# Kernel optimization log

Measured on AMD Instinct MI355X. Metric: run time of the kernel, lower is better.

## Reference

```python
import jax, jax.numpy as jnp
import numpy as np


def setup_inputs() -> dict:
    key = jax.random.key(0)
    k1, k2, k3 = jax.random.split(key, 3)
    C, H, W = 64, 512, 512
    D, K = 128, 3
    input = jax.random.normal(k1, (C, H, W), dtype=jnp.float32)
    # He-style init as in the module
    kernels = jax.random.normal(k2, (D, C, K, K), dtype=jnp.float32) * jnp.sqrt(2.0 / (C * K * K))
    biases = jax.random.normal(k3, (D, H - K + 1, W - K + 1), dtype=jnp.float32)
    return {"input": input, "kernels": kernels, "biases": biases}


def reference(input, kernels, biases):
    # valid 2D cross-correlation summed over input channels, plus per-pixel bias
    # input: [C,H,W], kernels: [D,C,k,k], biases: [D,H-k+1,W-k+1]
    x = input[None]  # [1,C,H,W]
    out = jax.lax.conv_general_dilated(
        x, kernels,
        window_strides=(1, 1),
        padding="VALID",
        dimension_numbers=("NCHW", "OIHW", "NCHW"),
    )[0]  # [D,H-k+1,W-k+1]; lax conv is cross-correlation, matching correlate2d
    return out + biases
```

## Files before the change

### kernel.cpp

```cpp
#include <hip/hip_runtime.h>
#include <hip/hip_bf16.h>

#define C_IN 64
#define H_IN 512
#define W_IN 512
#define D_OUT 128
#define OH 510
#define OW 510

typedef __bf16 bf16x8 __attribute__((ext_vector_type(8)));
typedef float  f32x4  __attribute__((ext_vector_type(4)));
typedef float  f32x2  __attribute__((ext_vector_type(2)));

#define TIN_ELEMS (H_IN * W_IN * C_IN)
#define TIN_BYTES ((size_t)TIN_ELEMS * 2)
#define WT_BYTES  (9 * D_OUT * C_IN * 2)
#define WS_NEEDED (TIN_BYTES + WT_BYTES)

__global__ void prep_weights(const float* __restrict__ w, __bf16* __restrict__ wt) {
    int i = blockIdx.x * blockDim.x + threadIdx.x;
    if (i >= 9 * D_OUT * C_IN) return;
    int c    = i & 63;
    int d    = (i >> 6) & 127;
    int kpos = i >> 13;
    wt[i] = (__bf16)w[((d * C_IN) + c) * 9 + kpos];
}

__global__ __launch_bounds__(256, 4)
void transpose_in(const float* __restrict__ in, __bf16* __restrict__ tin) {
    __shared__ float ls[32 * 257];
    const int b    = blockIdx.x;
    const int y    = b >> 1;
    const int px0  = (b & 1) << 8;
    const int t    = threadIdx.x;
    const int wave = t >> 6;
    const int lane = t & 63;

    for (int cc = 0; cc < 2; cc++) {
        if (cc) __syncthreads();
#pragma unroll
        for (int j = 0; j < 8; j++) {
            const int cl = wave * 8 + j;
            f32x4 v = *(const f32x4*)&in[(cc * 32 + cl) * (H_IN * W_IN) + y * W_IN + px0 + lane * 4];
            *(f32x4*)&ls[cl * 257 + lane * 4] = v;
        }
        __syncthreads();
        const int oct = t & 3;
        const int pxw = t >> 2;
#pragma unroll
        for (int pass = 0; pass < 4; pass++) {
            const int pxl = pass * 64 + pxw;
            bf16x8 v;
#pragma unroll
            for (int j = 0; j < 8; j++)
                v[j] = (__bf16)ls[(oct * 8 + j) * 257 + pxl];
            *(bf16x8*)&tin[((size_t)(y * W_IN) + px0 + pxl) * C_IN + cc * 32 + oct * 8] = v;
        }
    }
}

#define BPX 256
#define LO_STRIDE 260

__global__ __launch_bounds__(256, 4)
void conv_main(const __bf16* __restrict__ tin, const __bf16* __restrict__ wt,
               const float* __restrict__ bias, float* __restrict__ out) {
    __shared__ __align__(16) char smem[9 * 32 * 64 * 2];
    __bf16* lw = (__bf16*)smem;
    float*  lo = (float*)smem;

    const int b    = blockIdx.x;
    const int dt   = b & 3;
    const int xt   = (b >> 2) & 1;
    const int y    = b >> 3;
    const int d0   = dt << 5;
    const int x0   = xt ? (OW - BPX) : 0;

    const int t    = threadIdx.x;
    const int wave = t >> 6;
    const int lane = t & 63;
    const int l15  = lane & 15;
    const int quad = lane >> 4;

    {
        const int dl  = t >> 3, oc = t & 7;
        const int ocs = (oc ^ (dl & 7)) * 8;
#pragma unroll
        for (int kpos = 0; kpos < 9; kpos++) {
            bf16x8 v = *(const bf16x8*)(wt + kpos * (D_OUT * C_IN) + (d0 + dl) * C_IN + oc * 8);
            *(bf16x8*)&lw[(kpos * 32 + dl) * 64 + ocs] = v;
        }
    }
    __syncthreads();

    f32x2 bvals[16];
    const size_t ob = (size_t)(d0 + wave * 8) * (OH * OW) + (size_t)y * OW + x0 + lane * 4;
#pragma unroll
    for (int i = 0; i < 8; i++) {
        bvals[2 * i]     = *(const f32x2*)&bias[ob + (size_t)i * (OH * OW)];
        bvals[2 * i + 1] = *(const f32x2*)&bias[ob + (size_t)i * (OH * OW) + 2];
    }

    f32x4 acc[4][2];
#pragma unroll
    for (int pxg = 0; pxg < 4; pxg++)
#pragma unroll
        for (int dg = 0; dg < 2; dg++)
            acc[pxg][dg] = (f32x4){0.f, 0.f, 0.f, 0.f};

    const __bf16* tb = tin + ((size_t)y * W_IN + x0 + wave * 64) * C_IN + quad * 8;
#pragma unroll
    for (int kpos = 0; kpos < 9; kpos++) {
        const int ky = kpos / 3, kx = kpos % 3;
#pragma unroll
        for (int ch = 0; ch < 2; ch++) {
            const int us = (((ch * 4 + quad) ^ (l15 & 7)) * 8);
            bf16x8 w0 = *(const bf16x8*)&lw[(kpos * 32 + l15) * 64 + us];
            bf16x8 w1 = *(const bf16x8*)&lw[(kpos * 32 + 16 + l15) * 64 + us];
            const __bf16* base = tb + ((size_t)ky * W_IN + kx) * C_IN + ch * 32;
#pragma unroll
            for (int pxg = 0; pxg < 4; pxg++) {
                bf16x8 pf = *(const bf16x8*)(base + (pxg * 16 + l15) * C_IN);
                acc[pxg][0] = __builtin_amdgcn_mfma_f32_16x16x32_bf16(pf, w0, acc[pxg][0], 0, 0, 0);
                acc[pxg][1] = __builtin_amdgcn_mfma_f32_16x16x32_bf16(pf, w1, acc[pxg][1], 0, 0, 0);
            }
        }
    }

#pragma unroll
    for (int i = 0; i < 16; i++) asm volatile("" : "+v"(bvals[i]));

    __syncthreads();
#pragma unroll
    for (int pxg = 0; pxg < 4; pxg++)
#pragma unroll
        for (int dg = 0; dg < 2; dg++)
            *(f32x4*)&lo[(dg * 16 + l15) * LO_STRIDE + wave * 64 + pxg * 16 + quad * 4] = acc[pxg][dg];
    __syncthreads();
#pragma unroll
    for (int i = 0; i < 8; i++) {
        f32x4 v = *(const f32x4*)&lo[(wave * 8 + i) * LO_STRIDE + lane * 4];
        const size_t o = ob + (size_t)i * (OH * OW);
        f32x2 r0 = { v[0] + bvals[2 * i][0],     v[1] + bvals[2 * i][1] };
        f32x2 r1 = { v[2] + bvals[2 * i + 1][0], v[3] + bvals[2 * i + 1][1] };
        *(f32x2*)&out[o]     = r0;
        *(f32x2*)&out[o + 2] = r1;
    }
}

#define PXT 64
#define TCOL 66
#define TCPAD 72

__global__ __launch_bounds__(256, 4)
void conv_bias_fallback(const float* __restrict__ in, const __bf16* __restrict__ wt,
                        const float* __restrict__ bias, float* __restrict__ out) {
    __shared__ __bf16 tile[3 * TCOL * TCPAD];
    const int b  = blockIdx.x;
    const int y  = b >> 3;
    const int x0 = (b & 7) * PXT;
    const int tid = threadIdx.x;
    for (int idx = tid; idx < 3 * TCOL * C_IN; idx += 256) {
        int col = idx % TCOL;
        int t   = idx / TCOL;
        int r   = t % 3;
        int c   = t / 3;
        int gx  = x0 + col;
        if (gx > W_IN - 1) gx = W_IN - 1;
        tile[(r * TCOL + col) * TCPAD + c] = (__bf16)in[(c * H_IN + (y + r)) * W_IN + gx];
    }
    __syncthreads();
    const int wave = tid >> 6, lane = tid & 63;
    const int l15 = lane & 15, quad = lane >> 4;
    const int px_base = wave * 16;
    f32x4 acc[8];
#pragma unroll
    for (int i = 0; i < 8; i++) acc[i] = (f32x4){0.f, 0.f, 0.f, 0.f};
#pragma unroll
    for (int kpos = 0; kpos < 9; kpos++) {
        const int ky = kpos / 3, kx = kpos % 3;
#pragma unroll
        for (int ch = 0; ch < 2; ch++) {
            const int c0 = ch * 32;
            bf16x8 bfrag = *(const bf16x8*)&tile[(ky * TCOL + px_base + l15 + kx) * TCPAD + c0 + quad * 8];
            const __bf16* aptr = wt + (size_t)kpos * D_OUT * C_IN + l15 * C_IN + c0 + quad * 8;
#pragma unroll
            for (int ds = 0; ds < 8; ds++) {
                bf16x8 afrag = *(const bf16x8*)(aptr + ds * 16 * C_IN);
                acc[ds] = __builtin_amdgcn_mfma_f32_16x16x32_bf16(afrag, bfrag, acc[ds], 0, 0, 0);
            }
        }
    }
    const int gx = x0 + px_base + l15;
    if (gx < OW) {
#pragma unroll
        for (int ds = 0; ds < 8; ds++) {
            const int dbase = ds * 16 + quad * 4;
#pragma unroll
            for (int r = 0; r < 4; r++) {
                const size_t o = ((size_t)(dbase + r) * OH + y) * OW + gx;
                out[o] = acc[ds][r] + bias[o];
            }
        }
    }
}

extern "C" void kernel_launch(void* const* d_in, const int* in_sizes, int n_in,
                              void* d_out, int out_size, void* d_ws, size_t ws_size,
                              hipStream_t stream) {
    const float* in   = (const float*)d_in[0];
    const float* w    = (const float*)d_in[1];
    const float* bias = (const float*)d_in[2];
    float* out = (float*)d_out;

    if (ws_size >= WS_NEEDED) {
        __bf16* tin = (__bf16*)d_ws;
        __bf16* wt  = (__bf16*)((char*)d_ws + TIN_BYTES);
        prep_weights<<<(9 * D_OUT * C_IN + 255) / 256, 256, 0, stream>>>(w, wt);
        transpose_in<<<H_IN * 2, 256, 0, stream>>>(in, tin);
        conv_main<<<OH * 8, 256, 0, stream>>>(tin, wt, bias, out);
    } else {
        __bf16* wt = (__bf16*)d_ws;
        prep_weights<<<(9 * D_OUT * C_IN + 255) / 256, 256, 0, stream>>>(w, wt);
        conv_bias_fallback<<<OH * 8, 256, 0, stream>>>(in, wt, bias, out);
    }
}
```

Baseline: 416.6 us.

## Process two output rows per conv block and split transpose by channel half

conv_main now runs 512 threads covering two output rows, so the per-block weight staging into LDS is shared by twice as many pixels. Block indices are swizzled so neighbouring blocks land on different parts of the grid. The epilogue writes the two rows' results through LDS in two phases, with bias prefetched. transpose_in is split so each block handles one 32-channel half, doubling the grid and removing the inner loop and its barrier. The cost is more barriers in the epilogue and a larger block that may lower occupancy.

```diff
diff --git a/kernel.cpp b/kernel.cpp
--- a/kernel.cpp
+++ b/kernel.cpp
@@ -30,76 +30,69 @@
 void transpose_in(const float* __restrict__ in, __bf16* __restrict__ tin) {
     __shared__ float ls[32 * 257];
     const int b    = blockIdx.x;
-    const int y    = b >> 1;
-    const int px0  = (b & 1) << 8;
+    const int y    = b >> 2;
+    const int px0  = ((b >> 1) & 1) << 8;
+    const int cc   = b & 1;
     const int t    = threadIdx.x;
     const int wave = t >> 6;
     const int lane = t & 63;
 
-    for (int cc = 0; cc < 2; cc++) {
-        if (cc) __syncthreads();
-#pragma unroll
-        for (int j = 0; j < 8; j++) {
-            const int cl = wave * 8 + j;
-            f32x4 v = *(const f32x4*)&in[(cc * 32 + cl) * (H_IN * W_IN) + y * W_IN + px0 + lane * 4];
-            *(f32x4*)&ls[cl * 257 + lane * 4] = v;
-        }
-        __syncthreads();
-        const int oct = t & 3;
-        const int pxw = t >> 2;
-#pragma unroll
-        for (int pass = 0; pass < 4; pass++) {
-            const int pxl = pass * 64 + pxw;
-            bf16x8 v;
-#pragma unroll
-            for (int j = 0; j < 8; j++)
-                v[j] = (__bf16)ls[(oct * 8 + j) * 257 + pxl];
-            *(bf16x8*)&tin[((size_t)(y * W_IN) + px0 + pxl) * C_IN + cc * 32 + oct * 8] = v;
-        }
+#pragma unroll
+    for (int j = 0; j < 8; j++) {
+        const int cl = wave * 8 + j;
+        f32x4 v = *(const f32x4*)&in[(cc * 32 + cl) * (H_IN * W_IN) + y * W_IN + px0 + lane * 4];
+        *(f32x4*)&ls[cl * 257 + lane * 4] = v;
+    }
+    __syncthreads();
+    const int oct = t & 3;
+    const int pxw = t >> 2;
+#pragma unroll
+    for (int pass = 0; pass < 4; pass++) {
+        const int pxl = pass * 64 + pxw;
+        bf16x8 v;
+#pragma unroll
+        for (int j = 0; j < 8; j++)
+            v[j] = (__bf16)ls[(oct * 8 + j) * 257 + pxl];
+        *(bf16x8*)&tin[((size_t)(y * W_IN) + px0 + pxl) * C_IN + cc * 32 + oct * 8] = v;
     }
 }
 
 #define BPX 256
 #define LO_STRIDE 260
 
-__global__ __launch_bounds__(256, 4)
+__global__ __launch_bounds__(512, 6)
 void conv_main(const __bf16* __restrict__ tin, const __bf16* __restrict__ wt,
                const float* __restrict__ bias, float* __restrict__ out) {
     __shared__ __align__(16) char smem[9 * 32 * 64 * 2];
     __bf16* lw = (__bf16*)smem;
     float*  lo = (float*)smem;
 
-    const int b    = blockIdx.x;
-    const int dt   = b & 3;
-    const int xt   = (b >> 2) & 1;
-    const int y    = b >> 3;
-    const int d0   = dt << 5;
-    const int x0   = xt ? (OW - BPX) : 0;
+    const int bid = blockIdx.x;
+    const int swz = (bid & 7) * 255 + (bid >> 3);
+    const int dt  = swz & 3;
+    const int xt  = (swz >> 2) & 1;
+    const int y   = (swz >> 3) << 1;
+    const int d0  = dt << 5;
+    const int x0  = xt ? (OW - BPX) : 0;
 
     const int t    = threadIdx.x;
     const int wave = t >> 6;
     const int lane = t & 63;
     const int l15  = lane & 15;
     const int quad = lane >> 4;
-
-    {
-        const int dl  = t >> 3, oc = t & 7;
-        const int ocs = (oc ^ (dl & 7)) * 8;
-#pragma unroll
-        for (int kpos = 0; kpos < 9; kpos++) {
-            bf16x8 v = *(const bf16x8*)(wt + kpos * (D_OUT * C_IN) + (d0 + dl) * C_IN + oc * 8);
-            *(bf16x8*)&lw[(kpos * 32 + dl) * 64 + ocs] = v;
-        }
-    }
-    __syncthreads();
-
-    f32x2 bvals[16];
-    const size_t ob = (size_t)(d0 + wave * 8) * (OH * OW) + (size_t)y * OW + x0 + lane * 4;
-#pragma unroll
-    for (int i = 0; i < 8; i++) {
-        bvals[2 * i]     = *(const f32x2*)&bias[ob + (size_t)i * (OH * OW)];
-        bvals[2 * i + 1] = *(const f32x2*)&bias[ob + (size_t)i * (OH * OW) + 2];
-    }
+    const int wr   = wave >> 2;
+    const int wp   = wave & 3;
+
+    for (int u = t; u < 9 * 32 * 8; u += 512) {
+        const int kpos = u >> 8;
+        const int r    = u & 255;
+        const int dl   = r >> 3;
+        const int oc   = r & 7;
+        const int ocs  = (oc ^ (dl & 7)) * 8;
+        bf16x8 v = *(const bf16x8*)(wt + kpos * (D_OUT * C_IN) + (d0 + dl) * C_IN + oc * 8);
+        *(bf16x8*)&lw[(kpos * 32 + dl) * 64 + ocs] = v;
+    }
+    __syncthreads();
 
     f32x4 acc[4][2];
 #pragma unroll
@@ -108,7 +101,7 @@
         for (int dg = 0; dg < 2; dg++)
             acc[pxg][dg] = (f32x4){0.f, 0.f, 0.f, 0.f};
 
-    const __bf16* tb = tin + ((size_t)y * W_IN + x0 + wave * 64) * C_IN + quad * 8;
+    const __bf16* tb = tin + ((size_t)(y + wr) * W_IN + x0 + wp * 64) * C_IN + quad * 8;
 #pragma unroll
     for (int kpos = 0; kpos < 9; kpos++) {
         const int ky = kpos / 3, kx = kpos % 3;
@@ -127,22 +120,61 @@
         }
     }
 
-#pragma unroll
-    for (int i = 0; i < 16; i++) asm volatile("" : "+v"(bvals[i]));
-
-    __syncthreads();
-#pragma unroll
-    for (int pxg = 0; pxg < 4; pxg++)
-#pragma unroll
-        for (int dg = 0; dg < 2; dg++)
-            *(f32x4*)&lo[(dg * 16 + l15) * LO_STRIDE + wave * 64 + pxg * 16 + quad * 4] = acc[pxg][dg];
-    __syncthreads();
-#pragma unroll
-    for (int i = 0; i < 8; i++) {
-        f32x4 v = *(const f32x4*)&lo[(wave * 8 + i) * LO_STRIDE + lane * 4];
-        const size_t o = ob + (size_t)i * (OH * OW);
-        f32x2 r0 = { v[0] + bvals[2 * i][0],     v[1] + bvals[2 * i][1] };
-        f32x2 r1 = { v[2] + bvals[2 * i + 1][0], v[3] + bvals[2 * i + 1][1] };
+    const size_t OHW = (size_t)OH * OW;
+    const size_t obase = (size_t)(d0 + wave * 4) * OHW + (size_t)y * OW + x0 + lane * 4;
+    f32x2 bp[4][2];
+#pragma unroll
+    for (int i = 0; i < 4; i++) {
+        bp[i][0] = *(const f32x2*)&bias[obase + (size_t)i * OHW];
+        bp[i][1] = *(const f32x2*)&bias[obase + (size_t)i * OHW + 2];
+    }
+#pragma unroll
+    for (int i = 0; i < 4; i++) asm volatile("" : "+v"(bp[i][0]), "+v"(bp[i][1]));
+
+    __syncthreads();
+
+    if (wr == 0) {
+#pragma unroll
+        for (int pxg = 0; pxg < 4; pxg++)
+#pragma unroll
+            for (int dg = 0; dg < 2; dg++)
+                *(f32x4*)&lo[(dg * 16 + l15) * LO_STRIDE + wp * 64 + pxg * 16 + quad * 4] = acc[pxg][dg];
+    }
+    __syncthreads();
+
+    f32x2 bn[4][2];
+#pragma unroll
+    for (int i = 0; i < 4; i++) {
+        bn[i][0] = *(const f32x2*)&bias[obase + (size_t)i * OHW + OW];
+        bn[i][1] = *(const f32x2*)&bias[obase + (size_t)i * OHW + OW + 2];
+    }
+
+#pragma unroll
+    for (int i = 0; i < 4; i++) {
+        f32x4 v = *(const f32x4*)&lo[(wave * 4 + i) * LO_STRIDE + lane * 4];
+        const size_t o = obase + (size_t)i * OHW;
+        f32x2 r0 = { v[0] + bp[i][0][0], v[1] + bp[i][0][1] };
+        f32x2 r1 = { v[2] + bp[i][1][0], v[3] + bp[i][1][1] };
+        *(f32x2*)&out[o]     = r0;
+        *(f32x2*)&out[o + 2] = r1;
+    }
+    __syncthreads();
+
+    if (wr == 1) {
+#pragma unroll
+        for (int pxg = 0; pxg < 4; pxg++)
+#pragma unroll
+            for (int dg = 0; dg < 2; dg++)
+                *(f32x4*)&lo[(dg * 16 + l15) * LO_STRIDE + wp * 64 + pxg * 16 + quad * 4] = acc[pxg][dg];
+    }
+    __syncthreads();
+
+#pragma unroll
+    for (int i = 0; i < 4; i++) {
+        f32x4 v = *(const f32x4*)&lo[(wave * 4 + i) * LO_STRIDE + lane * 4];
+        const size_t o = obase + (size_t)i * OHW + OW;
+        f32x2 r0 = { v[0] + bn[i][0][0], v[1] + bn[i][0][1] };
+        f32x2 r1 = { v[2] + bn[i][1][0], v[3] + bn[i][1][1] };
         *(f32x2*)&out[o]     = r0;
         *(f32x2*)&out[o + 2] = r1;
     }
@@ -217,8 +249,8 @@
         __bf16* tin = (__bf16*)d_ws;
         __bf16* wt  = (__bf16*)((char*)d_ws + TIN_BYTES);
         prep_weights<<<(9 * D_OUT * C_IN + 255) / 256, 256, 0, stream>>>(w, wt);
-        transpose_in<<<H_IN * 2, 256, 0, stream>>>(in, tin);
-        conv_main<<<OH * 8, 256, 0, stream>>>(tin, wt, bias, out);
+        transpose_in<<<H_IN * 4, 256, 0, stream>>>(in, tin);
+        conv_main<<<(OH / 2) * 8, 512, 0, stream>>>(tin, wt, bias, out);
     } else {
         __bf16* wt = (__bf16*)d_ws;
         prep_weights<<<(9 * D_OUT * C_IN + 255) / 256, 256, 0, stream>>>(w, wt);
```

Result: no change. 418.9 us (+0.5%).
